# Kernel optimization log

Hardware: AMD Instinct MI355X
Metric: run time of the kernel (lower is better)

The kernel has to match this reference:

```python
import jax, jax.numpy as jnp
import numpy as np

D_MODEL = 1024
EXPAND = 2
D_INNER = D_MODEL * EXPAND  # 2048
D_STATE = 16
D_CONV = 4
B, T = 4, 2048


def setup_inputs() -> dict:
    key = jax.random.key(0)
    ks = jax.random.split(key, 8)
    s = 0.02  # small init std for numeric stability
    return {
        "x": jax.random.normal(ks[0], (B, T, D_MODEL), jnp.float32),
        "in_proj_w": jax.random.normal(ks[1], (2 * D_INNER, D_MODEL), jnp.float32) * s,
        "conv_w": jax.random.normal(ks[2], (D_INNER, 1, D_CONV), jnp.float32) * s,
        "conv_b": jnp.zeros((D_INNER,), jnp.float32),
        "x_proj_w": jax.random.normal(ks[3], (2 * D_STATE, D_INNER), jnp.float32) * s,
        "dt_proj_w": jax.random.normal(ks[4], (D_INNER, D_STATE), jnp.float32) * s,
        "dt_proj_b": jnp.zeros((D_INNER,), jnp.float32),
        "D_param": jnp.ones((D_INNER,), jnp.float32),
        "out_proj_w": jax.random.normal(ks[5], (D_MODEL, D_INNER), jnp.float32) * s,
    }


def reference(x, in_proj_w, conv_w, conv_b, x_proj_w, dt_proj_w, dt_proj_b, D_param, out_proj_w):
    Bsz, Tlen, _ = x.shape
    # in_proj (no bias), torch Linear: x @ W.T
    xz = jnp.einsum('btd,ed->bte', x, in_proj_w)            # [B,T,2*D_INNER]
    x_inner, z = jnp.split(xz, 2, axis=-1)                   # each [B,T,D_INNER]
    # depthwise causal conv1d: left-pad d_conv-1, take first T outputs
    xc = jnp.transpose(x_inner, (0, 2, 1))                   # [B,D_INNER,T]
    xc = jax.lax.conv_general_dilated(
        xc, conv_w, window_strides=(1,), padding=[(D_CONV - 1, 0)],
        feature_group_count=D_INNER)
    xc = xc + conv_b[None, :, None]
    x_conv = jax.nn.silu(jnp.transpose(xc, (0, 2, 1)))       # [B,T,D_INNER]
    # x_proj -> (B_ssm, C_ssm); C_ssm is unused by the simplified scan (faithful)
    x_ssm = jnp.einsum('btd,ed->bte', x_conv, x_proj_w)      # [B,T,2*D_STATE]
    B_ssm, C_ssm = jnp.split(x_ssm, 2, axis=-1)
    dt = jax.nn.softplus(jnp.einsum('btn,dn->btd', B_ssm, dt_proj_w) + dt_proj_b)  # [B,T,D_INNER]
    # simplified selective scan: EMA with scalar-per-timestep gate
    alpha = jax.nn.sigmoid(jnp.mean(dt, axis=-1, keepdims=True))  # [B,T,1]

    def step(h, inp):
        a, xt = inp
        h = a * h + (1.0 - a) * xt
        return h, h

    aT = jnp.transpose(alpha, (1, 0, 2))   # [T,B,1]
    xT = jnp.transpose(x_conv, (1, 0, 2))  # [T,B,D_INNER]
    h0 = jnp.zeros((Bsz, D_INNER), x.dtype)
    _, ys = jax.lax.scan(step, h0, (aT, xT))
    y = jnp.transpose(ys, (1, 0, 2))        # [B,T,D_INNER]
    y = y * D_param + x_conv                # skip with learned D
    y = y * jax.nn.silu(z)                  # gate
    out = jnp.einsum('btd,ed->bte', y, out_proj_w)  # [B,T,D_MODEL]
    return out
```

## Files before the change

### kernel.cpp

```cpp
#include <hip/hip_runtime.h>
#include <stdint.h>

#define TLEN   2048
#define DMODEL 1024
#define DINNER 2048
#define MROWS  8192
#define NCH    64
#define CHUNK  32

typedef unsigned short u16;
typedef __bf16 bf16x8 __attribute__((ext_vector_type(8)));
typedef float  f32x4  __attribute__((ext_vector_type(4)));

__device__ __forceinline__ float bf2f(u16 u) {
  union { unsigned int i; float f; } v; v.i = ((unsigned int)u) << 16; return v.f;
}
__device__ __forceinline__ u16 f2bf(float f) {
  union { float f; unsigned int u; } v; v.f = f;
  unsigned int u = v.u;
  return (u16)((u + 0x7fffu + ((u >> 16) & 1u)) >> 16);
}
__device__ __forceinline__ float silu_f(float x) { return x / (1.f + __expf(-x)); }

__device__ __forceinline__ void async16(const u16* g, u16* l) {
  __builtin_amdgcn_global_load_lds(
      (const __attribute__((address_space(1))) void*)(g),
      (__attribute__((address_space(3))) void*)(l),
      16, 0, 0);
}

#define BAR      asm volatile("s_barrier" ::: "memory")
#define WAITV(n) asm volatile("s_waitcnt vmcnt(" #n ")" ::: "memory")
#define PRIO1    __builtin_amdgcn_s_setprio(1)
#define PRIO0    __builtin_amdgcn_s_setprio(0)

__global__ __launch_bounds__(256) void k_convert(const float* __restrict__ x,
    const float* __restrict__ w1, const float* __restrict__ w3,
    const float* __restrict__ xpw,
    u16* __restrict__ xb, u16* __restrict__ w1b, u16* __restrict__ w3b,
    u16* __restrict__ xpwb) {
  int i = blockIdx.x * 256 + threadIdx.x;
  const int nx  = MROWS * DMODEL / 4;
  const int nw1 = 2 * DINNER * DMODEL / 4;
  const int nw3 = DMODEL * DINNER / 4;
  const float* src; u16* dst; int j;
  if (i < nx)                  { src = x;   dst = xb;   j = i; }
  else if (i < nx + nw1)       { src = w1;  dst = w1b;  j = i - nx; }
  else if (i < nx + nw1 + nw3) { src = w3;  dst = w3b;  j = i - nx - nw1; }
  else                         { src = xpw; dst = xpwb; j = i - nx - nw1 - nw3; }
  float4 v = ((const float4*)src)[j];
  ushort4 o;
  o.x = f2bf(v.x); o.y = f2bf(v.y); o.z = f2bf(v.z); o.w = f2bf(v.w);
  ((ushort4*)dst)[j] = o;
}

__device__ __forceinline__ u16* regp(u16* lds, int s, int mat, int h) {
  return lds + (((s * 2 + mat) * 2 + h) * 8192);
}

__device__ __forceinline__ void read_a(bf16x8 (&dst)[4][2], const u16* reg,
                                       int qa, int fr, int c0, int c1) {
  #pragma unroll
  for (int m = 0; m < 4; m++) {
    const u16* p = reg + (qa * 64 + m * 16 + fr) * 64;
    dst[m][0] = *(const bf16x8*)(p + c0);
    dst[m][1] = *(const bf16x8*)(p + c1);
  }
}
__device__ __forceinline__ void read_b(bf16x8 (&dst)[2][2], const u16* reg,
                                       int rb, int c0, int c1) {
  #pragma unroll
  for (int n = 0; n < 2; n++) {
    const u16* p = reg + (rb + n * 16) * 64;
    dst[n][0] = *(const bf16x8*)(p + c0);
    dst[n][1] = *(const bf16x8*)(p + c1);
  }
}
__device__ __forceinline__ void mfma_quad(f32x4 (&acc)[8][4],
    const bf16x8 (&af)[4][2], const bf16x8 (&bf)[2][2], int qa, int qb) {
  #pragma unroll
  for (int m = 0; m < 4; m++)
    #pragma unroll
    for (int n = 0; n < 2; n++)
      #pragma unroll
      for (int ks = 0; ks < 2; ks++)
        acc[qa * 4 + m][qb * 2 + n] = __builtin_amdgcn_mfma_f32_16x16x32_bf16(
            af[m][ks], bf[n][ks], acc[qa * 4 + m][qb * 2 + n], 0, 0, 0);
}

template<int N, int K, bool OUT_BF16>
__global__ __launch_bounds__(512) void k_gemm8p(const u16* __restrict__ A,
    const u16* __restrict__ Bm, void* __restrict__ C) {
  static_assert(K % 128 == 0, "K must be multiple of 128");
  extern __shared__ u16 lds[];
  const int tid  = threadIdx.x;
  const int lane = tid & 63;
  const int wave = tid >> 6;
  const int wm   = wave >> 2;
  const int wn   = wave & 3;
  const int fr   = lane & 15;
  const int q    = lane >> 4;

  int wg = blockIdx.x, nwg = gridDim.x, swz = wg;
  if ((nwg & 7) == 0) swz = (wg & 7) * (nwg >> 3) + (wg >> 3);
  const int NT_N = N / 256;
  const size_t blockM = (size_t)(swz / NT_N) * 256;
  const size_t blockN = (size_t)(swz % NT_N) * 256;

  const int rsub   = tid >> 3;
  const int srcCol = 8 * ((tid & 7) ^ (rsub & 7));
  const u16* gA = A  + (blockM + rsub) * (size_t)K + srcCol;
  const u16* gB = Bm + (blockN + rsub) * (size_t)K + srcCol;

#define STAGE(sl, mat, h, kt) do {                                           \
    const u16* _g = ((mat) ? gB : gA) + (size_t)(h) * (128 * (size_t)K)      \
                    + (size_t)(kt) * 64;                                     \
    u16* _l = regp(lds, (sl), (mat), (h)) + tid * 8;                         \
    async16(_g, _l);                                                         \
    async16(_g + (size_t)64 * K, _l + 4096);                                 \
  } while (0)

  const int c0 = (((q * 16)      ^ ((fr & 7) << 4)) >> 1);
  const int c1 = (((64 + q * 16) ^ ((fr & 7) << 4)) >> 1);
  const int rb = (wn & 1) * 64 + fr;

  f32x4 acc[8][4] = {};
  bf16x8 a0[4][2], a1[4][2], bl[2][2], bh[2][2];

  const int NT = K / 64;
  const int NITER = K / 128;

  STAGE(0, 0, 0, 0); STAGE(0, 0, 1, 0); STAGE(0, 1, 0, 0); STAGE(0, 1, 1, 0);
  STAGE(1, 1, 0, 1); STAGE(1, 1, 1, 1); STAGE(1, 0, 0, 1);
  WAITV(6);
  BAR;

  for (int it = 0; it < NITER; ++it) {
    const int t2 = 2 * it + 2, t3 = 2 * it + 3;
    const bool pf = (t2 < NT);
    read_a(a0, regp(lds, 0, 0, wm), 0, fr, c0, c1);
    read_b(bl, regp(lds, 0, 1, wn >> 1), rb, c0, c1);
    STAGE(1, 0, 1, 2 * it + 1);
    BAR;
    PRIO1; mfma_quad(acc, a0, bl, 0, 0); PRIO0;
    BAR;
    read_b(bh, regp(lds, 0, 1, wn >> 1), rb + 32, c0, c1);
    if (pf) STAGE(0, 1, 0, t2);
    BAR;
    PRIO1; mfma_quad(acc, a0, bh, 0, 1); PRIO0;
    BAR;
    read_a(a1, regp(lds, 0, 0, wm), 1, fr, c0, c1);
    if (pf) STAGE(0, 1, 1, t2);
    BAR;
    PRIO1; mfma_quad(acc, a1, bl, 1, 0); PRIO0;
    BAR;
    if (pf) STAGE(0, 0, 0, t2);
    BAR;
    PRIO1; mfma_quad(acc, a1, bh, 1, 1); PRIO0;
    if (pf) { WAITV(6); } else { WAITV(0); }
    BAR;
    read_a(a0, regp(lds, 1, 0, wm), 0, fr, c0, c1);
    read_b(bl, regp(lds, 1, 1, wn >> 1), rb, c0, c1);
    if (pf) STAGE(0, 0, 1, t2);
    BAR;
    PRIO1; mfma_quad(acc, a0, bl, 0, 0); PRIO0;
    BAR;
    read_b(bh, regp(lds, 1, 1, wn >> 1), rb + 32, c0, c1);
    if (pf) STAGE(1, 1, 0, t3);
    BAR;
    PRIO1; mfma_quad(acc, a0, bh, 0, 1); PRIO0;
    BAR;
    read_a(a1, regp(lds, 1, 0, wm), 1, fr, c0, c1);
    if (pf) STAGE(1, 1, 1, t3);
    BAR;
    PRIO1; mfma_quad(acc, a1, bl, 1, 0); PRIO0;
    BAR;
    if (pf) STAGE(1, 0, 0, t3);
    BAR;
    PRIO1; mfma_quad(acc, a1, bh, 1, 1); PRIO0;
    if (pf) { WAITV(6); BAR; } else { BAR; }
  }
#undef STAGE

  {
    const size_t r0  = blockM + (size_t)wm * 128;
    const size_t cc0 = blockN + (size_t)wn * 64;
    #pragma unroll
    for (int m = 0; m < 8; m++)
      #pragma unroll
      for (int n = 0; n < 4; n++)
        #pragma unroll
        for (int r = 0; r < 4; r++) {
          size_t row = r0 + m * 16 + q * 4 + r;
          size_t col = cc0 + n * 16 + fr;
          float v = acc[m][n][r];
          if (OUT_BF16) ((u16*)C)[row * N + col] = f2bf(v);
          else          ((float*)C)[row * N + col] = v;
        }
  }
}

template<int N, int K, bool OUT_BF16>
__global__ __launch_bounds__(512) void k_gemm_sk(const u16* __restrict__ A,
    const u16* __restrict__ B, void* __restrict__ C) {
  __shared__ u16 smem[2][2][2][4096];
  const int tid   = threadIdx.x;
  const int lane  = tid & 63;
  const int wave8 = tid >> 6;
  const int kw    = wave8 >> 2;
  const int wave  = wave8 & 3;
  const int wm    = (wave >> 1) * 64;
  const int wn    = (wave & 1) * 64;
  const int fr    = lane & 15;
  const int q     = lane >> 4;
  const size_t blockM = (size_t)blockIdx.y * 128;
  const size_t blockN = (size_t)blockIdx.x * 128;

  const int srow = lane >> 2;
  const int scol = (lane & 3) * 8;
  const size_t kbase = (size_t)kw * (K / 2);
  const u16* gA = A + (blockM + (size_t)wave * 32 + srow) * (size_t)K + kbase + scol;
  const u16* gB = B + (blockN + (size_t)wave * 32 + srow) * (size_t)K + kbase + scol;
  u16* lA0 = smem[kw][0][0] + wave * 1024;
  u16* lA1 = smem[kw][0][1] + wave * 1024;
  u16* lB0 = smem[kw][1][0] + wave * 1024;
  u16* lB1 = smem[kw][1][1] + wave * 1024;

  f32x4 acc[4][4] = {};

  for (int kt = 0; kt < K / 2; kt += 64) {
    async16(gA + kt,                        lA0);
    async16(gA + 16 * (size_t)K + kt,       lA0 + 512);
    async16(gA + kt + 32,                   lA1);
    async16(gA + 16 * (size_t)K + kt + 32,  lA1 + 512);
    async16(gB + kt,                        lB0);
    async16(gB + 16 * (size_t)K + kt,       lB0 + 512);
    async16(gB + kt + 32,                   lB1);
    async16(gB + 16 * (size_t)K + kt + 32,  lB1 + 512);
    __syncthreads();

    #pragma unroll
    for (int h = 0; h < 2; h++) {
      bf16x8 af[4], bfr[4];
      #pragma unroll
      for (int tm = 0; tm < 4; tm++)
        af[tm] = *(const bf16x8*)(smem[kw][0][h] + (wm + tm * 16 + fr) * 32 + q * 8);
      #pragma unroll
      for (int tn = 0; tn < 4; tn++)
        bfr[tn] = *(const bf16x8*)(smem[kw][1][h] + (wn + tn * 16 + fr) * 32 + q * 8);
      #pragma unroll
      for (int tm = 0; tm < 4; tm++)
        #pragma unroll
        for (int tn = 0; tn < 4; tn++)
          acc[tm][tn] = __builtin_amdgcn_mfma_f32_16x16x32_bf16(
              af[tm], bfr[tn], acc[tm][tn], 0, 0, 0);
    }
    __syncthreads();
  }

  float* red = (float*)smem;
  if (kw == 1) {
    const int t2 = tid - 256;
    #pragma unroll
    for (int tm = 0; tm < 4; tm++)
      #pragma unroll
      for (int tn = 0; tn < 4; tn++)
        #pragma unroll
        for (int r = 0; r < 4; r++)
          red[((t2 * 4 + tm) * 4 + tn) * 4 + r] = acc[tm][tn][r];
  }
  __syncthreads();
  if (kw == 0) {
    #pragma unroll
    for (int tm = 0; tm < 4; tm++)
      #pragma unroll
      for (int tn = 0; tn < 4; tn++)
        #pragma unroll
        for (int r = 0; r < 4; r++) {
          float v = acc[tm][tn][r] + red[((tid * 4 + tm) * 4 + tn) * 4 + r];
          size_t row = blockM + wm + tm * 16 + q * 4 + r;
          size_t col = blockN + wn + tn * 16 + fr;
          if (OUT_BF16) ((u16*)C)[row * N + col] = f2bf(v);
          else          ((float*)C)[row * N + col] = v;
        }
  }
}

__global__ __launch_bounds__(256) void k_conv(const u16* __restrict__ xz,
    const float* __restrict__ cw, const float* __restrict__ cb,
    u16* __restrict__ xc) {
  const int tb = blockIdx.x & 255;
  const int b  = blockIdx.x >> 8;
  const int d0 = threadIdx.x * 8;

  float wgt[8][4], bias[8];
  #pragma unroll
  for (int j = 0; j < 8; j++) {
    float4 wv = ((const float4*)cw)[d0 + j];
    wgt[j][0] = wv.x; wgt[j][1] = wv.y; wgt[j][2] = wv.z; wgt[j][3] = wv.w;
    bias[j] = cb[d0 + j];
  }

  const int t0 = tb * 8;
  const u16* base = xz + ((size_t)(b * TLEN + t0)) * 4096 + d0;
  float win[3][8];
  #pragma unroll
  for (int k = 0; k < 3; k++) {
    const int t = t0 - 3 + k;
    if (t >= 0) {
      bf16x8 v = *(const bf16x8*)(base + (ptrdiff_t)(k - 3) * 4096);
      #pragma unroll
      for (int j = 0; j < 8; j++) win[k][j] = bf2f(((u16*)&v)[j]);
    } else {
      #pragma unroll
      for (int j = 0; j < 8; j++) win[k][j] = 0.f;
    }
  }

  u16* outp = xc + ((size_t)(b * TLEN + t0)) * DINNER + d0;
  #pragma unroll
  for (int i = 0; i < 8; i++) {
    bf16x8 v = *(const bf16x8*)(base + (ptrdiff_t)i * 4096);
    float cur[8];
    #pragma unroll
    for (int j = 0; j < 8; j++) cur[j] = bf2f(((u16*)&v)[j]);
    union { u16 a[8]; int4 v4; } o;
    #pragma unroll
    for (int j = 0; j < 8; j++) {
      float acc = bias[j] + wgt[j][0] * win[0][j] + wgt[j][1] * win[1][j]
                + wgt[j][2] * win[2][j] + wgt[j][3] * cur[j];
      o.a[j] = f2bf(silu_f(acc));
    }
    *(int4*)(outp + (size_t)i * DINNER) = o.v4;
    #pragma unroll
    for (int j = 0; j < 8; j++) { win[0][j] = win[1][j]; win[1][j] = win[2][j]; win[2][j] = cur[j]; }
  }
}

__global__ __launch_bounds__(256) void k_bssm(const u16* __restrict__ xc,
    const u16* __restrict__ xpwb, float* __restrict__ bssm) {
  const int tid  = threadIdx.x;
  const int lane = tid & 63;
  const int wave = tid >> 6;
  const int fr   = lane & 15;
  const int q    = lane >> 4;
  const size_t row0 = (size_t)blockIdx.x * 32;
  const int k0 = wave * 512;

  f32x4 acc[2] = {};
  #pragma unroll
  for (int kk = 0; kk < 512; kk += 32) {
    const int kb = k0 + kk + q * 8;
    bf16x8 bfrag = *(const bf16x8*)(xpwb + (size_t)fr * DINNER + kb);
    #pragma unroll
    for (int tm = 0; tm < 2; tm++) {
      bf16x8 afrag = *(const bf16x8*)(xc + (row0 + tm * 16 + fr) * (size_t)DINNER + kb);
      acc[tm] = __builtin_amdgcn_mfma_f32_16x16x32_bf16(afrag, bfrag, acc[tm], 0, 0, 0);
    }
  }

  __shared__ float red[4][32][16];
  #pragma unroll
  for (int tm = 0; tm < 2; tm++)
    #pragma unroll
    for (int r = 0; r < 4; r++)
      red[wave][tm * 16 + q * 4 + r][fr] = acc[tm][r];
  __syncthreads();
  #pragma unroll
  for (int i = tid; i < 512; i += 256) {
    int r = i >> 4, n = i & 15;
    bssm[(row0 + r) * 16 + n] =
        red[0][r][n] + red[1][r][n] + red[2][r][n] + red[3][r][n];
  }
}

__global__ __launch_bounds__(256) void k_alpha(const float* __restrict__ bssm,
    const float* __restrict__ dtw, const float* __restrict__ dtb,
    float* __restrict__ alpha) {
  const int tid = threadIdx.x;
  const size_t row0 = (size_t)blockIdx.x * 16;
  __shared__ float4 sB[16][4];
  { int r = tid >> 4, n = tid & 15;
    ((float*)&sB[r][0])[n] = bssm[(row0 + r) * 16 + n]; }
  __syncthreads();

  float rowsum[16];
  #pragma unroll
  for (int r = 0; r < 16; r++) rowsum[r] = 0.f;

  #pragma unroll 1
  for (int m = 0; m < 4; m++) {
    const int d0 = m * 512 + tid * 2;
    float4 w[2][4]; float bias[2];
    #pragma unroll
    for (int j = 0; j < 2; j++) {
      const float4* wp = (const float4*)(dtw + (size_t)(d0 + j) * 16);
      w[j][0] = wp[0]; w[j][1] = wp[1]; w[j][2] = wp[2]; w[j][3] = wp[3];
      bias[j] = dtb[d0 + j];
    }
    #pragma unroll
    for (int r = 0; r < 16; r++) {
      float4 b0 = sB[r][0], b1 = sB[r][1], b2 = sB[r][2], b3 = sB[r][3];
      float s = 0.f;
      #pragma unroll
      for (int j = 0; j < 2; j++) {
        float dot = bias[j]
          + b0.x * w[j][0].x + b0.y * w[j][0].y + b0.z * w[j][0].z + b0.w * w[j][0].w
          + b1.x * w[j][1].x + b1.y * w[j][1].y + b1.z * w[j][1].z + b1.w * w[j][1].w
          + b2.x * w[j][2].x + b2.y * w[j][2].y + b2.z * w[j][2].z + b2.w * w[j][2].w
          + b3.x * w[j][3].x + b3.y * w[j][3].y + b3.z * w[j][3].z + b3.w * w[j][3].w;
        s += (dot > 15.f) ? dot : __logf(1.f + __expf(dot));
      }
      rowsum[r] += s;
    }
  }
  #pragma unroll
  for (int r = 0; r < 16; r++)
    #pragma unroll
    for (int off = 32; off > 0; off >>= 1) rowsum[r] += __shfl_xor(rowsum[r], off);
  __shared__ float red[4][16];
  if ((tid & 63) == 0) {
    #pragma unroll
    for (int r = 0; r < 16; r++) red[tid >> 6][r] = rowsum[r];
  }
  __syncthreads();
  if (tid < 16) {
    float mean = (red[0][tid] + red[1][tid] + red[2][tid] + red[3][tid]) * (1.f / DINNER);
    alpha[row0 + tid] = 1.f / (1.f + __expf(-mean));
  }
}

__global__ __launch_bounds__(256) void k_scan1(const u16* __restrict__ xc,
    const float* __restrict__ alpha, float* __restrict__ carry) {
  const int c = blockIdx.x & 63;
  const int b = blockIdx.x >> 6;
  const int d0 = threadIdx.x * 8;
  __shared__ float sa[CHUNK];
  if (threadIdx.x < CHUNK) sa[threadIdx.x] = alpha[b * TLEN + c * CHUNK + threadIdx.x];
  __syncthreads();
  const u16* xp = xc + ((size_t)(b * TLEN + c * CHUNK)) * DINNER + d0;
  float h[8];
  #pragma unroll
  for (int j = 0; j < 8; j++) h[j] = 0.f;
  #pragma unroll 4
  for (int i = 0; i < CHUNK; i++) {
    bf16x8 v = *(const bf16x8*)(xp + (size_t)i * DINNER);
    float a = sa[i];
    #pragma unroll
    for (int j = 0; j < 8; j++) h[j] = a * h[j] + (1.f - a) * bf2f(((u16*)&v)[j]);
  }
  float* cp = carry + ((size_t)(b * NCH + c)) * DINNER + d0;
  #pragma unroll
  for (int j = 0; j < 8; j++) cp[j] = h[j];
}

__global__ __launch_bounds__(256) void k_scan2(float* __restrict__ carry,
    const float* __restrict__ alpha) {
  int i = blockIdx.x * 256 + threadIdx.x;
  int b = i >> 11;
  int d = i & (DINNER - 1);
  __shared__ float sP[NCH];
  if (threadIdx.x < NCH) {
    const float* ap = alpha + b * TLEN + threadIdx.x * CHUNK;
    float p = 1.f;
    for (int j = 0; j < CHUNK; j++) p *= ap[j];
    sP[threadIdx.x] = p;
  }
  __syncthreads();
  float h = 0.f;
  #pragma unroll
  for (int c = 0; c < NCH; c++) {
    size_t idx = ((size_t)(b * NCH + c)) * DINNER + d;
    float cv = carry[idx];
    carry[idx] = h;
    h = sP[c] * h + cv;
  }
}

__global__ __launch_bounds__(256) void k_scan3(const u16* __restrict__ xc,
    const u16* __restrict__ xz, const float* __restrict__ alpha,
    const float* __restrict__ Hs, const float* __restrict__ Dp,
    u16* __restrict__ yg) {
  const int c = blockIdx.x & 63;
  const int b = blockIdx.x >> 6;
  const int d0 = threadIdx.x * 8;
  __shared__ float sa[CHUNK];
  if (threadIdx.x < CHUNK) sa[threadIdx.x] = alpha[b * TLEN + c * CHUNK + threadIdx.x];
  __syncthreads();
  float h[8], Dv[8];
  { const float* hp = Hs + ((size_t)(b * NCH + c)) * DINNER + d0;
    #pragma unroll
    for (int j = 0; j < 8; j++) { h[j] = hp[j]; Dv[j] = Dp[d0 + j]; } }
  const size_t row0 = (size_t)(b * TLEN + c * CHUNK);
  #pragma unroll 2
  for (int i = 0; i < CHUNK; i++) {
    const size_t row = row0 + i;
    bf16x8 xv8 = *(const bf16x8*)(xc + row * DINNER + d0);
    bf16x8 zv8 = *(const bf16x8*)(xz + row * 4096 + DINNER + d0);
    const float a = sa[i];
    union { u16 o[8]; int4 v4; } out;
    #pragma unroll
    for (int j = 0; j < 8; j++) {
      float xv = bf2f(((u16*)&xv8)[j]);
      float zv = bf2f(((u16*)&zv8)[j]);
      h[j] = a * h[j] + (1.f - a) * xv;
      float y = h[j] * Dv[j] + xv;
      out.o[j] = f2bf(y * silu_f(zv));
    }
    *(int4*)(yg + row * DINNER + d0) = out.v4;
  }
}

extern "C" void kernel_launch(void* const* d_in, const int* in_sizes, int n_in,
                              void* d_out, int out_size, void* d_ws, size_t ws_size,
                              hipStream_t stream) {
  const float* x   = (const float*)d_in[0];
  const float* w1  = (const float*)d_in[1];
  const float* cw  = (const float*)d_in[2];
  const float* cb  = (const float*)d_in[3];
  const float* xpw = (const float*)d_in[4];
  const float* dtw = (const float*)d_in[5];
  const float* dtb = (const float*)d_in[6];
  const float* Dp  = (const float*)d_in[7];
  const float* w3  = (const float*)d_in[8];
  float* out = (float*)d_out;
  char* ws = (char*)d_ws;

  u16*   xb    = (u16*)(ws + 0);
  u16*   w1b   = (u16*)(ws + 16777216);
  u16*   w3b   = (u16*)(ws + 25165824);
  u16*   xz    = (u16*)(ws + 29360128);
  u16*   xc    = (u16*)(ws + 96468992);
  u16*   yg    = (u16*)(ws + 130023424);
  float* bssm  = (float*)(ws + 163577856);
  float* alpha = (float*)(ws + 164102144);
  float* carry = (float*)(ws + 0);
  u16*   xpwb  = (u16*)(ws + 164659456);

  k_convert<<<14368, 256, 0, stream>>>(x, w1, w3, xpw, xb, w1b, w3b, xpwb);
  k_gemm8p<4096, 1024, true><<<512, 512, 131072, stream>>>(xb, w1b, xz);
  k_conv   <<<1024, 256, 0, stream>>>(xz, cw, cb, xc);
  k_bssm   <<<256, 256, 0, stream>>>(xc, xpwb, bssm);
  k_alpha  <<<512, 256, 0, stream>>>(bssm, dtw, dtb, alpha);
  k_scan1  <<<256, 256, 0, stream>>>(xc, alpha, carry);
  k_scan2  <<<32, 256, 0, stream>>>(carry, alpha);
  k_scan3  <<<256, 256, 0, stream>>>(xc, xz, alpha, carry, Dp, yg);
  k_gemm_sk<1024, 2048, false><<<dim3(8, 64), 512, 0, stream>>>(yg, w3b, out);
}
```

Baseline: 327.7 us.

## Fuse bssm/alpha/scan1 kernels, retile output GEMM, split scan3 across more blocks

Merges the B_ssm projection, the dt/softplus/mean/sigmoid alpha computation and the first chunk-scan pass into one kernel, which also emits per-chunk alpha products for scan2. This removes two launches and the intermediate bssm round trip. The output GEMM drops split-K in favour of 128x64 tiles on 256-thread blocks (1024 blocks), and scan3 uses twice as many blocks with 4 channels per thread. The fused kernel runs the dt projection on only 256 blocks with a long serial loop per thread, which may cost more than the launches it removes.

After: 379.4 us. 1.16x slower.

```diff
diff --git a/kernel.cpp b/kernel.cpp
--- a/kernel.cpp
+++ b/kernel.cpp
@@ -200,90 +200,70 @@
   }
 }
 
-template<int N, int K, bool OUT_BF16>
-__global__ __launch_bounds__(512) void k_gemm_sk(const u16* __restrict__ A,
-    const u16* __restrict__ B, void* __restrict__ C) {
-  __shared__ u16 smem[2][2][2][4096];
-  const int tid   = threadIdx.x;
-  const int lane  = tid & 63;
-  const int wave8 = tid >> 6;
-  const int kw    = wave8 >> 2;
-  const int wave  = wave8 & 3;
-  const int wm    = (wave >> 1) * 64;
-  const int wn    = (wave & 1) * 64;
-  const int fr    = lane & 15;
-  const int q     = lane >> 4;
+template<int N, int K>
+__global__ __launch_bounds__(256) void k_gemm2(const u16* __restrict__ A,
+    const u16* __restrict__ B, float* __restrict__ C) {
+  __shared__ u16 sA[2][128 * 32];
+  __shared__ u16 sB[2][64 * 32];
+  const int tid  = threadIdx.x;
+  const int lane = tid & 63;
+  const int wave = tid >> 6;
+  const int wm   = (wave >> 1) * 64;
+  const int wn   = (wave & 1) * 32;
+  const int fr   = lane & 15;
+  const int q    = lane >> 4;
   const size_t blockM = (size_t)blockIdx.y * 128;
-  const size_t blockN = (size_t)blockIdx.x * 128;
+  const size_t blockN = (size_t)blockIdx.x * 64;
 
   const int srow = lane >> 2;
   const int scol = (lane & 3) * 8;
-  const size_t kbase = (size_t)kw * (K / 2);
-  const u16* gA = A + (blockM + (size_t)wave * 32 + srow) * (size_t)K + kbase + scol;
-  const u16* gB = B + (blockN + (size_t)wave * 32 + srow) * (size_t)K + kbase + scol;
-  u16* lA0 = smem[kw][0][0] + wave * 1024;
-  u16* lA1 = smem[kw][0][1] + wave * 1024;
-  u16* lB0 = smem[kw][1][0] + wave * 1024;
-  u16* lB1 = smem[kw][1][1] + wave * 1024;
-
-  f32x4 acc[4][4] = {};
-
-  for (int kt = 0; kt < K / 2; kt += 64) {
+  const u16* gA = A + (blockM + (size_t)wave * 32 + srow) * (size_t)K + scol;
+  const u16* gB = B + (blockN + (size_t)wave * 16 + srow) * (size_t)K + scol;
+  u16* lA0 = sA[0] + wave * 1024;
+  u16* lA1 = sA[1] + wave * 1024;
+  u16* lB0 = sB[0] + wave * 512;
+  u16* lB1 = sB[1] + wave * 512;
+
+  f32x4 acc[4][2] = {};
+
+  for (int kt = 0; kt < K; kt += 64) {
     async16(gA + kt,                        lA0);
     async16(gA + 16 * (size_t)K + kt,       lA0 + 512);
     async16(gA + kt + 32,                   lA1);
     async16(gA + 16 * (size_t)K + kt + 32,  lA1 + 512);
     async16(gB + kt,                        lB0);
-    async16(gB + 16 * (size_t)K + kt,       lB0 + 512);
     async16(gB + kt + 32,                   lB1);
-    async16(gB + 16 * (size_t)K + kt + 32,  lB1 + 512);
     __syncthreads();
 
     #pragma unroll
     for (int h = 0; h < 2; h++) {
-      bf16x8 af[4], bfr[4];
+      bf16x8 af[4], bfr[2];
       #pragma unroll
       for (int tm = 0; tm < 4; tm++)
-        af[tm] = *(const bf16x8*)(smem[kw][0][h] + (wm + tm * 16 + fr) * 32 + q * 8);
-      #pragma unroll
-      for (int tn = 0; tn < 4; tn++)
-        bfr[tn] = *(const bf16x8*)(smem[kw][1][h] + (wn + tn * 16 + fr) * 32 + q * 8);
+        af[tm] = *(const bf16x8*)(sA[h] + (wm + tm * 16 + fr) * 32 + q * 8);
+      #pragma unroll
+      for (int tn = 0; tn < 2; tn++)
+        bfr[tn] = *(const bf16x8*)(sB[h] + (wn + tn * 16 + fr) * 32 + q * 8);
       #pragma unroll
       for (int tm = 0; tm < 4; tm++)
         #pragma unroll
-        for (int tn = 0; tn < 4; tn++)
+        for (int tn = 0; tn < 2; tn++)
           acc[tm][tn] = __builtin_amdgcn_mfma_f32_16x16x32_bf16(
               af[tm], bfr[tn], acc[tm][tn], 0, 0, 0);
     }
     __syncthreads();
   }
 
-  float* red = (float*)smem;
-  if (kw == 1) {
-    const int t2 = tid - 256;
-    #pragma unroll
-    for (int tm = 0; tm < 4; tm++)
-      #pragma unroll
-      for (int tn = 0; tn < 4; tn++)
-        #pragma unroll
-        for (int r = 0; r < 4; r++)
-          red[((t2 * 4 + tm) * 4 + tn) * 4 + r] = acc[tm][tn][r];
-  }
-  __syncthreads();
-  if (kw == 0) {
-    #pragma unroll
-    for (int tm = 0; tm < 4; tm++)
-      #pragma unroll
-      for (int tn = 0; tn < 4; tn++)
-        #pragma unroll
-        for (int r = 0; r < 4; r++) {
-          float v = acc[tm][tn][r] + red[((tid * 4 + tm) * 4 + tn) * 4 + r];
-          size_t row = blockM + wm + tm * 16 + q * 4 + r;
-          size_t col = blockN + wn + tn * 16 + fr;
-          if (OUT_BF16) ((u16*)C)[row * N + col] = f2bf(v);
-          else          ((float*)C)[row * N + col] = v;
-        }
-  }
+  #pragma unroll
+  for (int tm = 0; tm < 4; tm++)
+    #pragma unroll
+    for (int tn = 0; tn < 2; tn++)
+      #pragma unroll
+      for (int r = 0; r < 4; r++) {
+        size_t row = blockM + wm + tm * 16 + q * 4 + r;
+        size_t col = blockN + wn + tn * 16 + fr;
+        C[row * N + col] = acc[tm][tn][r];
+      }
 }
 
 __global__ __launch_bounds__(256) void k_conv(const u16* __restrict__ xz,
@@ -337,8 +317,10 @@
   }
 }
 
-__global__ __launch_bounds__(256) void k_bssm(const u16* __restrict__ xc,
-    const u16* __restrict__ xpwb, float* __restrict__ bssm) {
+__global__ __launch_bounds__(256) void k_fused(const u16* __restrict__ xc,
+    const u16* __restrict__ xpwb, const float* __restrict__ dtw,
+    const float* __restrict__ dtb, float* __restrict__ alpha,
+    float* __restrict__ Pprod, float* __restrict__ carry) {
   const int tid  = threadIdx.x;
   const int lane = tid & 63;
   const int wave = tid >> 6;
@@ -358,7 +340,6 @@
       acc[tm] = __builtin_amdgcn_mfma_f32_16x16x32_bf16(afrag, bfrag, acc[tm], 0, 0, 0);
     }
   }
-
   __shared__ float red[4][32][16];
   #pragma unroll
   for (int tm = 0; tm < 2; tm++)
@@ -366,114 +347,87 @@
     for (int r = 0; r < 4; r++)
       red[wave][tm * 16 + q * 4 + r][fr] = acc[tm][r];
   __syncthreads();
-  #pragma unroll
+  __shared__ float sBs[32][16];
   for (int i = tid; i < 512; i += 256) {
     int r = i >> 4, n = i & 15;
-    bssm[(row0 + r) * 16 + n] =
-        red[0][r][n] + red[1][r][n] + red[2][r][n] + red[3][r][n];
-  }
-}
-
-__global__ __launch_bounds__(256) void k_alpha(const float* __restrict__ bssm,
-    const float* __restrict__ dtw, const float* __restrict__ dtb,
-    float* __restrict__ alpha) {
-  const int tid = threadIdx.x;
-  const size_t row0 = (size_t)blockIdx.x * 16;
-  __shared__ float4 sB[16][4];
-  { int r = tid >> 4, n = tid & 15;
-    ((float*)&sB[r][0])[n] = bssm[(row0 + r) * 16 + n]; }
+    sBs[r][n] = red[0][r][n] + red[1][r][n] + red[2][r][n] + red[3][r][n];
+  }
   __syncthreads();
 
-  float rowsum[16];
-  #pragma unroll
-  for (int r = 0; r < 16; r++) rowsum[r] = 0.f;
-
-  #pragma unroll 1
-  for (int m = 0; m < 4; m++) {
-    const int d0 = m * 512 + tid * 2;
-    float4 w[2][4]; float bias[2];
-    #pragma unroll
-    for (int j = 0; j < 2; j++) {
-      const float4* wp = (const float4*)(dtw + (size_t)(d0 + j) * 16);
-      w[j][0] = wp[0]; w[j][1] = wp[1]; w[j][2] = wp[2]; w[j][3] = wp[3];
-      bias[j] = dtb[d0 + j];
-    }
-    #pragma unroll
-    for (int r = 0; r < 16; r++) {
-      float4 b0 = sB[r][0], b1 = sB[r][1], b2 = sB[r][2], b3 = sB[r][3];
-      float s = 0.f;
-      #pragma unroll
-      for (int j = 0; j < 2; j++) {
-        float dot = bias[j]
-          + b0.x * w[j][0].x + b0.y * w[j][0].y + b0.z * w[j][0].z + b0.w * w[j][0].w
-          + b1.x * w[j][1].x + b1.y * w[j][1].y + b1.z * w[j][1].z + b1.w * w[j][1].w
-          + b2.x * w[j][2].x + b2.y * w[j][2].y + b2.z * w[j][2].z + b2.w * w[j][2].w
-          + b3.x * w[j][3].x + b3.y * w[j][3].y + b3.z * w[j][3].z + b3.w * w[j][3].w;
-        s += (dot > 15.f) ? dot : __logf(1.f + __expf(dot));
-      }
-      rowsum[r] += s;
-    }
-  }
-  #pragma unroll
-  for (int r = 0; r < 16; r++)
-    #pragma unroll
-    for (int off = 32; off > 0; off >>= 1) rowsum[r] += __shfl_xor(rowsum[r], off);
-  __shared__ float red[4][16];
-  if ((tid & 63) == 0) {
-    #pragma unroll
-    for (int r = 0; r < 16; r++) red[tid >> 6][r] = rowsum[r];
+  __shared__ float sA2[32];
+  {
+    const int r  = tid >> 3;
+    const int ds = tid & 7;
+    float4 b0 = *(const float4*)&sBs[r][0];
+    float4 b1 = *(const float4*)&sBs[r][4];
+    float4 b2 = *(const float4*)&sBs[r][8];
+    float4 b3 = *(const float4*)&sBs[r][12];
+    float s = 0.f;
+    for (int k = 0; k < 256; k++) {
+      const int d = ds + k * 8;
+      const float4* wp = (const float4*)(dtw + (size_t)d * 16);
+      float4 w0 = wp[0], w1 = wp[1], w2 = wp[2], w3 = wp[3];
+      float dot = dtb[d]
+        + b0.x * w0.x + b0.y * w0.y + b0.z * w0.z + b0.w * w0.w
+        + b1.x * w1.x + b1.y * w1.y + b1.z * w1.z + b1.w * w1.w
+        + b2.x * w2.x + b2.y * w2.y + b2.z * w2.z + b2.w * w2.w
+        + b3.x * w3.x + b3.y * w3.y + b3.z * w3.z + b3.w * w3.w;
+      s += (dot > 15.f) ? dot : __logf(1.f + __expf(dot));
+    }
+    s += __shfl_xor(s, 1); s += __shfl_xor(s, 2); s += __shfl_xor(s, 4);
+    if (ds == 0) sA2[r] = s;
   }
   __syncthreads();
-  if (tid < 16) {
-    float mean = (red[0][tid] + red[1][tid] + red[2][tid] + red[3][tid]) * (1.f / DINNER);
-    alpha[row0 + tid] = 1.f / (1.f + __expf(-mean));
-  }
-}
-
-__global__ __launch_bounds__(256) void k_scan1(const u16* __restrict__ xc,
-    const float* __restrict__ alpha, float* __restrict__ carry) {
-  const int c = blockIdx.x & 63;
-  const int b = blockIdx.x >> 6;
-  const int d0 = threadIdx.x * 8;
-  __shared__ float sa[CHUNK];
-  if (threadIdx.x < CHUNK) sa[threadIdx.x] = alpha[b * TLEN + c * CHUNK + threadIdx.x];
+  if (tid < 32) {
+    float mean = sA2[tid] * (1.f / DINNER);
+    float a = 1.f / (1.f + __expf(-mean));
+    sA2[tid] = a;
+    alpha[row0 + tid] = a;
+  }
   __syncthreads();
-  const u16* xp = xc + ((size_t)(b * TLEN + c * CHUNK)) * DINNER + d0;
-  float h[8];
-  #pragma unroll
-  for (int j = 0; j < 8; j++) h[j] = 0.f;
-  #pragma unroll 4
-  for (int i = 0; i < CHUNK; i++) {
-    bf16x8 v = *(const bf16x8*)(xp + (size_t)i * DINNER);
-    float a = sa[i];
-    #pragma unroll
-    for (int j = 0; j < 8; j++) h[j] = a * h[j] + (1.f - a) * bf2f(((u16*)&v)[j]);
-  }
-  float* cp = carry + ((size_t)(b * NCH + c)) * DINNER + d0;
-  #pragma unroll
-  for (int j = 0; j < 8; j++) cp[j] = h[j];
+  if (tid == 0) {
+    float p = 1.f;
+    #pragma unroll
+    for (int i = 0; i < 32; i++) p *= sA2[i];
+    Pprod[blockIdx.x] = p;
+  }
+
+  {
+    const int d0 = tid * 8;
+    float h[8];
+    #pragma unroll
+    for (int j = 0; j < 8; j++) h[j] = 0.f;
+    const u16* xp = xc + row0 * DINNER + d0;
+    for (int i = 0; i < 32; i++) {
+      bf16x8 v = *(const bf16x8*)(xp + (size_t)i * DINNER);
+      float a = sA2[i];
+      #pragma unroll
+      for (int j = 0; j < 8; j++)
+        h[j] = a * h[j] + (1.f - a) * bf2f(((u16*)&v)[j]);
+    }
+    float* cp = carry + (size_t)blockIdx.x * DINNER + d0;
+    #pragma unroll
+    for (int j = 0; j < 8; j++) cp[j] = h[j];
+  }
 }
 
 __global__ __launch_bounds__(256) void k_scan2(float* __restrict__ carry,
-    const float* __restrict__ alpha) {
+    const float* __restrict__ Pprod) {
   int i = blockIdx.x * 256 + threadIdx.x;
   int b = i >> 11;
   int d = i & (DINNER - 1);
   __shared__ float sP[NCH];
-  if (threadIdx.x < NCH) {
-    const float* ap = alpha + b * TLEN + threadIdx.x * CHUNK;
-    float p = 1.f;
-    for (int j = 0; j < CHUNK; j++) p *= ap[j];
-    sP[threadIdx.x] = p;
-  }
+  if (threadIdx.x < NCH) sP[threadIdx.x] = Pprod[b * NCH + threadIdx.x];
   __syncthreads();
+  float* base = carry + (size_t)b * NCH * DINNER + d;
+  float cv[NCH];
+  #pragma unroll
+  for (int c = 0; c < NCH; c++) cv[c] = base[(size_t)c * DINNER];
   float h = 0.f;
   #pragma unroll
   for (int c = 0; c < NCH; c++) {
-    size_t idx = ((size_t)(b * NCH + c)) * DINNER + d;
-    float cv = carry[idx];
-    carry[idx] = h;
-    h = sP[c] * h + cv;
+    base[(size_t)c * DINNER] = h;
+    h = sP[c] * h + cv[c];
   }
 }
 
@@ -481,33 +435,36 @@
     const u16* __restrict__ xz, const float* __restrict__ alpha,
     const float* __restrict__ Hs, const float* __restrict__ Dp,
     u16* __restrict__ yg) {
-  const int c = blockIdx.x & 63;
-  const int b = blockIdx.x >> 6;
-  const int d0 = threadIdx.x * 8;
+  const int half = blockIdx.x & 1;
+  const int c = (blockIdx.x >> 1) & 63;
+  const int b = blockIdx.x >> 7;
+  const int d0 = half * 1024 + threadIdx.x * 4;
   __shared__ float sa[CHUNK];
   if (threadIdx.x < CHUNK) sa[threadIdx.x] = alpha[b * TLEN + c * CHUNK + threadIdx.x];
   __syncthreads();
-  float h[8], Dv[8];
+  float h[4], Dv[4];
   { const float* hp = Hs + ((size_t)(b * NCH + c)) * DINNER + d0;
     #pragma unroll
-    for (int j = 0; j < 8; j++) { h[j] = hp[j]; Dv[j] = Dp[d0 + j]; } }
+    for (int j = 0; j < 4; j++) { h[j] = hp[j]; Dv[j] = Dp[d0 + j]; } }
   const size_t row0 = (size_t)(b * TLEN + c * CHUNK);
   #pragma unroll 2
   for (int i = 0; i < CHUNK; i++) {
     const size_t row = row0 + i;
-    bf16x8 xv8 = *(const bf16x8*)(xc + row * DINNER + d0);
-    bf16x8 zv8 = *(const bf16x8*)(xz + row * 4096 + DINNER + d0);
+    ushort4 xv4 = *(const ushort4*)(xc + row * DINNER + d0);
+    ushort4 zv4 = *(const ushort4*)(xz + row * 4096 + DINNER + d0);
     const float a = sa[i];
-    union { u16 o[8]; int4 v4; } out;
-    #pragma unroll
-    for (int j = 0; j < 8; j++) {
-      float xv = bf2f(((u16*)&xv8)[j]);
-      float zv = bf2f(((u16*)&zv8)[j]);
-      h[j] = a * h[j] + (1.f - a) * xv;
-      float y = h[j] * Dv[j] + xv;
-      out.o[j] = f2bf(y * silu_f(zv));
-    }
-    *(int4*)(yg + row * DINNER + d0) = out.v4;
+    union { u16 o[4]; uint2 v2; } out;
+    const u16* xv = (const u16*)&xv4;
+    const u16* zv = (const u16*)&zv4;
+    #pragma unroll
+    for (int j = 0; j < 4; j++) {
+      float x = bf2f(xv[j]);
+      float z = bf2f(zv[j]);
+      h[j] = a * h[j] + (1.f - a) * x;
+      float y = h[j] * Dv[j] + x;
+      out.o[j] = f2bf(y * silu_f(z));
+    }
+    *(uint2*)(yg + row * DINNER + d0) = out.v2;
   }
 }
 
@@ -532,7 +489,7 @@
   u16*   xz    = (u16*)(ws + 29360128);
   u16*   xc    = (u16*)(ws + 96468992);
   u16*   yg    = (u16*)(ws + 130023424);
-  float* bssm  = (float*)(ws + 163577856);
+  float* Pprod = (float*)(ws + 163577856);
   float* alpha = (float*)(ws + 164102144);
   float* carry = (float*)(ws + 0);
   u16*   xpwb  = (u16*)(ws + 164659456);
@@ -540,10 +497,8 @@
   k_convert<<<14368, 256, 0, stream>>>(x, w1, w3, xpw, xb, w1b, w3b, xpwb);
   k_gemm8p<4096, 1024, true><<<512, 512, 131072, stream>>>(xb, w1b, xz);
   k_conv   <<<1024, 256, 0, stream>>>(xz, cw, cb, xc);
-  k_bssm   <<<256, 256, 0, stream>>>(xc, xpwb, bssm);
-  k_alpha  <<<512, 256, 0, stream>>>(bssm, dtw, dtb, alpha);
-  k_scan1  <<<256, 256, 0, stream>>>(xc, alpha, carry);
-  k_scan2  <<<32, 256, 0, stream>>>(carry, alpha);
-  k_scan3  <<<256, 256, 0, stream>>>(xc, xz, alpha, carry, Dp, yg);
-  k_gemm_sk<1024, 2048, false><<<dim3(8, 64), 512, 0, stream>>>(yg, w3b, out);
-}
+  k_fused  <<<256, 256, 0, stream>>>(xc, xpwb, dtw, dtb, alpha, Pprod, carry);
+  k_scan2  <<<32, 256, 0, stream>>>(carry, Pprod);
+  k_scan3  <<<512, 256, 0, stream>>>(xc, xz, alpha, carry, Dp, yg);
+  k_gemm2<1024, 2048><<<dim3(16, 64), 256, 0, stream>>>(yg, w3b, out);
+}
```
